# Optimization experiments

Hardware: AMD Instinct MI355X
Metric: run time of the kernel (lower is better)

## Reference

```python
import jax, jax.numpy as jnp
import numpy as np

B, F, V, D = 4096, 8, 1000, 1024  # batch, n_fields, vocab per field, hidden_size
LN_EPS = 1e-5


def layer_norm(x, g, b, eps=LN_EPS):
    mu = x.mean(axis=-1, keepdims=True)
    var = ((x - mu) ** 2).mean(axis=-1, keepdims=True)
    return (x - mu) * jax.lax.rsqrt(var + eps) * g + b


def setup_inputs() -> dict:
    key = jax.random.key(0)
    k0, k1, k2, k3 = jax.random.split(key, 4)
    return {
        "input_embedding": jax.random.normal(k0, (B, D), jnp.float32),
        "features": jax.random.randint(k1, (B, F), 0, V),
        "embed_tables": jax.random.normal(k2, (F, V, D), jnp.float32) * 0.02,
        "ln_gamma": jnp.ones((D,), jnp.float32),
        "ln_beta": jnp.zeros((D,), jnp.float32),
        "pred_W": jax.random.normal(k3, (F, D, V), jnpp := jnp.float32) * 0.02,
        "pred_b": jnp.zeros((F, V), jnp.float32),
    }


def reference(input_embedding, features, embed_tables, ln_gamma, ln_beta, pred_W, pred_b):
    # Per-field embedding lookup: (B, F, D)
    feat_emb = embed_tables[jnp.arange(F)[None, :], features]
    # Stack input embedding first, as in torch.stack([input_embedding] + ...):
    embeddings = jnp.concatenate([input_embedding[:, None, :], feat_emb], axis=1)  # (B, F+1, D)
    # triu(diagonal=1) masked broadcast-sum then [:, 1:, :] == exclusive causal prefix sum:
    # masked_sums[:, j] = sum_{i < j+1} embeddings[:, i] for j = 0..F-1
    masked_sums = jnp.cumsum(embeddings, axis=1)[:, :F, :]  # (B, F, D)
    h = jax.nn.gelu(layer_norm(masked_sums, ln_gamma, ln_beta), approximate=False)
    # Per-field predictor heads (Linear(D, V)), batched over fields:
    logits = jnp.einsum("bfd,fdv->bfv", h, pred_W) + pred_b  # (B, F, V)
    return logits
```

## Files before the change

kernel.cpp:

```cpp
#include <hip/hip_runtime.h>
#include <hip/hip_bf16.h>

#define B_ 4096
#define F_ 8
#define V_ 1000
#define D_ 1024
#define VP 1024

typedef __bf16 bf16x8 __attribute__((ext_vector_type(8)));
typedef float f32x4 __attribute__((ext_vector_type(4)));

__device__ __forceinline__ void gload_lds16(const void* g, void* l) {
  __builtin_amdgcn_global_load_lds(
      (const __attribute__((address_space(1))) void*)g,
      (__attribute__((address_space(3))) void*)l, 16, 0, 0);
}

__global__ __launch_bounds__(256) void transpose_w(
    const float* __restrict__ W, __hip_bfloat16* __restrict__ Wt) {
  __shared__ float tile[32][33];
  const int f = blockIdx.z;
  const int k0 = blockIdx.x * 32;
  const int v0 = blockIdx.y * 32;
  const int tx = threadIdx.x;
  const int ty = threadIdx.y;
  const float* Wf = W + (size_t)f * D_ * V_;
#pragma unroll
  for (int i = 0; i < 4; ++i) {
    int k = k0 + ty + i * 8;
    int v = v0 + tx;
    tile[ty + i * 8][tx] = (v < V_) ? Wf[k * V_ + v] : 0.0f;
  }
  __syncthreads();
  __hip_bfloat16* Wtf = Wt + (size_t)f * VP * D_;
#pragma unroll
  for (int i = 0; i < 4; ++i) {
    int v = v0 + ty + i * 8;
    int k = k0 + tx;
    Wtf[v * D_ + k] = __float2bfloat16(tile[tx][ty + i * 8]);
  }
}

__global__ __launch_bounds__(256) void fuse_h(
    const float* __restrict__ emb, const int* __restrict__ feats,
    const float* __restrict__ tables, const float* __restrict__ gamma,
    const float* __restrict__ beta, __hip_bfloat16* __restrict__ H) {
  const int b = blockIdx.x;
  const int t = threadIdx.x;
  const int d = t * 4;
  const int wave = t >> 6, lane = t & 63;

  float s[4];
  {
    float4 v = *reinterpret_cast<const float4*>(&emb[(size_t)b * D_ + d]);
    s[0] = v.x; s[1] = v.y; s[2] = v.z; s[3] = v.w;
  }
  float gm[4], bt[4];
  {
    float4 g = *reinterpret_cast<const float4*>(&gamma[d]);
    float4 bb = *reinterpret_cast<const float4*>(&beta[d]);
    gm[0] = g.x; gm[1] = g.y; gm[2] = g.z; gm[3] = g.w;
    bt[0] = bb.x; bt[1] = bb.y; bt[2] = bb.z; bt[3] = bb.w;
  }
  __shared__ float red[2][4][2];

  for (int f = 0; f < F_; ++f) {
    float sum = s[0] + s[1] + s[2] + s[3];
    float ssq = s[0] * s[0] + s[1] * s[1] + s[2] * s[2] + s[3] * s[3];
#pragma unroll
    for (int off = 32; off > 0; off >>= 1) {
      sum += __shfl_xor(sum, off, 64);
      ssq += __shfl_xor(ssq, off, 64);
    }
    const int pb = f & 1;
    if (lane == 0) { red[pb][wave][0] = sum; red[pb][wave][1] = ssq; }
    __syncthreads();
    sum = red[pb][0][0] + red[pb][1][0] + red[pb][2][0] + red[pb][3][0];
    ssq = red[pb][0][1] + red[pb][1][1] + red[pb][2][1] + red[pb][3][1];

    const float mu = sum * (1.0f / D_);
    const float var = ssq * (1.0f / D_) - mu * mu;
    const float rstd = rsqrtf(var + 1e-5f);

    __hip_bfloat16 hb[4];
#pragma unroll
    for (int j = 0; j < 4; ++j) {
      float x = (s[j] - mu) * rstd * gm[j] + bt[j];
      float g = 0.5f * x * (1.0f + erff(x * 0.70710678118654752f));
      hb[j] = __float2bfloat16(g);
    }
    *reinterpret_cast<uint2*>(&H[(size_t)f * (B_ * D_) + (size_t)b * D_ + d]) =
        *reinterpret_cast<const uint2*>(hb);

    if (f < F_ - 1) {
      int feat = feats[b * F_ + f];
      const float* row = tables + ((size_t)f * V_ + feat) * D_;
      float4 tv = *reinterpret_cast<const float4*>(&row[d]);
      s[0] += tv.x; s[1] += tv.y; s[2] += tv.z; s[3] += tv.w;
    }
  }
}

#define STAGE(ARR, GB, HALF, KT)                                              \
  do {                                                                        \
    const ushort* _g = (GB) + (size_t)(HALF) * (128 * D_) + (size_t)(KT) * 64;\
    ushort* _l = &ARR[(HALF)*8192 + w * 512];                                 \
    gload_lds16(_g, _l);                                                      \
    gload_lds16(_g + 64 * D_, _l + 4096);                                     \
  } while (0)

#define LD_A(DST, LBASE, FIOFF)                                               \
  _Pragma("unroll") for (int _fj = 0; _fj < 4; ++_fj)                         \
  _Pragma("unroll") for (int _ks = 0; _ks < 2; ++_ks)                         \
      DST[_fj][_ks] = *reinterpret_cast<const bf16x8*>(                       \
          (LBASE) + ((((FIOFF) + _fj) * 2 + _ks) * 512));

#define LD_B(DST, LBASE, NFOFF)                                               \
  _Pragma("unroll") for (int _fn = 0; _fn < 2; ++_fn)                         \
  _Pragma("unroll") for (int _ks = 0; _ks < 2; ++_ks)                         \
      DST[_fn][_ks] = *reinterpret_cast<const bf16x8*>(                       \
          (LBASE) + ((((NFOFF) + _fn) * 2 + _ks) * 512));

#define Q_MFMA(AF, BF, R0, C0)                                                \
  do {                                                                        \
    __builtin_amdgcn_s_setprio(1);                                            \
    _Pragma("unroll") for (int _fj = 0; _fj < 4; ++_fj)                       \
    _Pragma("unroll") for (int _fn = 0; _fn < 2; ++_fn)                       \
    _Pragma("unroll") for (int _ks = 0; _ks < 2; ++_ks)                       \
        acc[(R0) + _fj][(C0) + _fn] =                                         \
            __builtin_amdgcn_mfma_f32_16x16x32_bf16(                          \
                AF[_fj][_ks], BF[_fn][_ks], acc[(R0) + _fj][(C0) + _fn],      \
                0, 0, 0);                                                     \
    __builtin_amdgcn_s_setprio(0);                                            \
  } while (0)

#define BAR __builtin_amdgcn_s_barrier()
#define SB0 __builtin_amdgcn_sched_barrier(0)
#define VM4 asm volatile("s_waitcnt vmcnt(4)")
#define VM0 asm volatile("s_waitcnt vmcnt(0)")
#define LG0 asm volatile("s_waitcnt lgkmcnt(0)")

__global__ __launch_bounds__(512, 2) void gemm_hw(
    const ushort* __restrict__ H,
    const ushort* __restrict__ Wt,
    const float* __restrict__ bias,
    float* __restrict__ out) {
  __shared__ ushort Ad0[16384];
  __shared__ ushort Ad1[16384];
  __shared__ ushort Bd0[16384];
  __shared__ ushort Bd1[16384];

  const int bid = blockIdx.x;
  const int swz = (bid & 7) * 64 + (bid >> 3);
  const int f = swz >> 6;
  const int r = swz & 63;
  const int mt = r >> 2, nt = r & 3;

  const int t = threadIdx.x;
  const int w = t >> 6, l = t & 63;
  const int wm = w >> 2;
  const int wn = w & 3;

  const ushort* Hf = H + (size_t)f * (B_ * D_);
  const ushort* Wf = Wt + (size_t)f * (VP * D_);

  const int srow = ((w >> 1) << 4) + (l >> 2);
  const int skx = ((w & 1) << 5) + ((((l & 3) << 3)) ^ (((l >> 5) & 1) << 4));
  const ushort* gA = Hf + (size_t)(mt * 256 + srow) * D_ + skx;
  const ushort* gB = Wf + (size_t)(nt * 256 + srow) * D_ + skx;

  const int laneu =
      ((l & 15) << 5) + (((((l >> 4) << 4)) ^ (((l >> 3) & 1) << 5)) >> 1);
  const ushort* lA[2] = {&Ad0[wm * 8192 + laneu], &Ad1[wm * 8192 + laneu]};
  const ushort* lB[2] = {&Bd0[(wn >> 1) * 8192 + (wn & 1) * 4096 + laneu],
                         &Bd1[(wn >> 1) * 8192 + (wn & 1) * 4096 + laneu]};

  bf16x8 a0[4][2], a1[4][2], b0[2][2], b1[2][2];
  f32x4 acc[8][4] = {};

  STAGE(Ad0, gA, 0, 0);
  STAGE(Ad0, gA, 1, 0);
  STAGE(Bd0, gB, 0, 0);
  STAGE(Bd0, gB, 1, 0);
  STAGE(Ad1, gA, 0, 1);
  STAGE(Ad1, gA, 1, 1);
  VM4;
  BAR;

#pragma unroll 1
  for (int i = 0; i < 8; ++i) {
    const int t1 = 2 * i + 1, t2 = 2 * i + 2, t3 = 2 * i + 3;
    const bool more = (i < 7);
    LD_A(a0, lA[0], 0);
    LD_B(b0, lB[0], 0);
    STAGE(Bd1, gB, 0, t1);
    BAR;
    LG0;
    SB0;
    Q_MFMA(a0, b0, 0, 0);
    LD_A(a1, lA[0], 4);
    STAGE(Bd1, gB, 1, t1);
    BAR;
    LG0;
    SB0;
    Q_MFMA(a1, b0, 4, 0);
    LD_B(b1, lB[0], 2);
    if (more) STAGE(Ad0, gA, 0, t2);
    BAR;
    LG0;
    SB0;
    Q_MFMA(a0, b1, 0, 2);
    if (more) {
      STAGE(Ad0, gA, 1, t2);
      VM4;
    } else {
      VM0;
    }
    BAR;
    SB0;
    Q_MFMA(a1, b1, 4, 2);
    LD_A(a0, lA[1], 0);
    LD_B(b0, lB[1], 0);
    if (more) STAGE(Bd0, gB, 0, t2);
    BAR;
    LG0;
    SB0;
    Q_MFMA(a0, b0, 0, 0);
    LD_A(a1, lA[1], 4);
    if (more) STAGE(Bd0, gB, 1, t2);
    BAR;
    LG0;
    SB0;
    Q_MFMA(a1, b0, 4, 0);
    LD_B(b1, lB[1], 2);
    if (more) STAGE(Ad1, gA, 0, t3);
    BAR;
    LG0;
    SB0;
    Q_MFMA(a0, b1, 0, 2);
    if (more) {
      STAGE(Ad1, gA, 1, t3);
      VM4;
    }
    BAR;
    SB0;
    Q_MFMA(a1, b1, 4, 2);
  }

  const float* bp = bias + f * V_;
  const int orow0 = mt * 256 + wm * 128 + ((l >> 4) << 2);
  const int ocol0 = nt * 256 + wn * 64 + (l & 15);
#pragma unroll
  for (int fi = 0; fi < 8; ++fi) {
#pragma unroll
    for (int fn = 0; fn < 4; ++fn) {
      int col = ocol0 + fn * 16;
      if (col < V_) {
        float bb = bp[col];
        int row = orow0 + fi * 16;
        float* op = out + (size_t)row * (F_ * V_) + (size_t)f * V_ + col;
#pragma unroll
        for (int q = 0; q < 4; ++q)
          op[(size_t)q * (F_ * V_)] = acc[fi][fn][q] + bb;
      }
    }
  }
}

extern "C" void kernel_launch(void* const* d_in, const int* in_sizes, int n_in,
                              void* d_out, int out_size, void* d_ws,
                              size_t ws_size, hipStream_t stream) {
  const float* emb = (const float*)d_in[0];
  const int* feats = (const int*)d_in[1];
  const float* tables = (const float*)d_in[2];
  const float* gamma = (const float*)d_in[3];
  const float* beta = (const float*)d_in[4];
  const float* W = (const float*)d_in[5];
  const float* bias = (const float*)d_in[6];
  float* out = (float*)d_out;

  char* ws = (char*)d_ws;
  __hip_bfloat16* Hbuf = (__hip_bfloat16*)ws;
  __hip_bfloat16* Wtbuf =
      (__hip_bfloat16*)(ws + (size_t)F_ * B_ * D_ * 2);

  transpose_w<<<dim3(D_ / 32, VP / 32, F_), dim3(32, 8), 0, stream>>>(W, Wtbuf);
  fuse_h<<<dim3(B_), dim3(256), 0, stream>>>(emb, feats, tables, gamma, beta,
                                             Hbuf);
  gemm_hw<<<dim3((B_ / 256) * (VP / 256) * F_), dim3(512), 0, stream>>>(
      (const ushort*)Hbuf, (const ushort*)Wtbuf, bias, out);
}
```

Before: 137.2 us.

## Software-pipeline LDS fragment loads against MFMAs and prefetch embedding rows

In the GEMM main loop, the LDS reads of the next A/B fragments now start before the current MFMA group rather than after it. The explicit lgkmcnt(0) waits are removed, so the compiler places the LDS waits and the reads can overlap matrix math. The first fragments are loaded before the loop, and each iteration prefetches the next iteration's fragments. In fuse_h, all seven embedding-table rows are loaded up front so their latency is not paid serially inside the field loop. The cost is higher register pressure in both kernels and more reliance on the correctness of the barrier and sched_barrier ordering.

```diff
diff --git a/kernel.cpp b/kernel.cpp
--- a/kernel.cpp
+++ b/kernel.cpp
@@ -55,6 +55,13 @@
     float4 v = *reinterpret_cast<const float4*>(&emb[(size_t)b * D_ + d]);
     s[0] = v.x; s[1] = v.y; s[2] = v.z; s[3] = v.w;
   }
+  float4 tv[7];
+#pragma unroll
+  for (int j = 0; j < 7; ++j) {
+    int feat = feats[b * F_ + j];
+    tv[j] = *reinterpret_cast<const float4*>(
+        &tables[((size_t)j * V_ + feat) * D_ + d]);
+  }
   float gm[4], bt[4];
   {
     float4 g = *reinterpret_cast<const float4*>(&gamma[d]);
@@ -93,10 +100,7 @@
         *reinterpret_cast<const uint2*>(hb);
 
     if (f < F_ - 1) {
-      int feat = feats[b * F_ + f];
-      const float* row = tables + ((size_t)f * V_ + feat) * D_;
-      float4 tv = *reinterpret_cast<const float4*>(&row[d]);
-      s[0] += tv.x; s[1] += tv.y; s[2] += tv.z; s[3] += tv.w;
+      s[0] += tv[f].x; s[1] += tv[f].y; s[2] += tv[f].z; s[3] += tv[f].w;
     }
   }
 }
@@ -138,7 +142,6 @@
 #define SB0 __builtin_amdgcn_sched_barrier(0)
 #define VM4 asm volatile("s_waitcnt vmcnt(4)")
 #define VM0 asm volatile("s_waitcnt vmcnt(0)")
-#define LG0 asm volatile("s_waitcnt lgkmcnt(0)")
 
 __global__ __launch_bounds__(512, 2) void gemm_hw(
     const ushort* __restrict__ H,
@@ -186,28 +189,28 @@
   STAGE(Ad1, gA, 1, 1);
   VM4;
   BAR;
+  LD_A(a0, lA[0], 0);
+  LD_B(b0, lB[0], 0);
+  SB0;
 
 #pragma unroll 1
   for (int i = 0; i < 8; ++i) {
     const int t1 = 2 * i + 1, t2 = 2 * i + 2, t3 = 2 * i + 3;
     const bool more = (i < 7);
-    LD_A(a0, lA[0], 0);
-    LD_B(b0, lB[0], 0);
     STAGE(Bd1, gB, 0, t1);
     BAR;
-    LG0;
+    SB0;
+    LD_A(a1, lA[0], 4);
     SB0;
     Q_MFMA(a0, b0, 0, 0);
-    LD_A(a1, lA[0], 4);
     STAGE(Bd1, gB, 1, t1);
     BAR;
-    LG0;
+    SB0;
+    LD_B(b1, lB[0], 2);
     SB0;
     Q_MFMA(a1, b0, 4, 0);
-    LD_B(b1, lB[0], 2);
     if (more) STAGE(Ad0, gA, 0, t2);
     BAR;
-    LG0;
     SB0;
     Q_MFMA(a0, b1, 0, 2);
     if (more) {
@@ -218,24 +221,24 @@
     }
     BAR;
     SB0;
-    Q_MFMA(a1, b1, 4, 2);
     LD_A(a0, lA[1], 0);
     LD_B(b0, lB[1], 0);
+    SB0;
+    Q_MFMA(a1, b1, 4, 2);
     if (more) STAGE(Bd0, gB, 0, t2);
     BAR;
-    LG0;
+    SB0;
+    LD_A(a1, lA[1], 4);
     SB0;
     Q_MFMA(a0, b0, 0, 0);
-    LD_A(a1, lA[1], 4);
     if (more) STAGE(Bd0, gB, 1, t2);
     BAR;
-    LG0;
+    SB0;
+    LD_B(b1, lB[1], 2);
     SB0;
     Q_MFMA(a1, b0, 4, 0);
-    LD_B(b1, lB[1], 2);
     if (more) STAGE(Ad1, gA, 0, t3);
     BAR;
-    LG0;
     SB0;
     Q_MFMA(a0, b1, 0, 2);
     if (more) {
@@ -243,6 +246,11 @@
       VM4;
     }
     BAR;
+    SB0;
+    if (more) {
+      LD_A(a0, lA[0], 0);
+      LD_B(b0, lB[0], 0);
+    }
     SB0;
     Q_MFMA(a1, b1, 4, 2);
   }
```

New measurement: 139.4 us. Within noise of the previous version (+1.6%).
